# Optimization experiments

Measured on AMD Instinct MI355X. Metric: run time of the kernel, lower is better.

The kernel has to match this reference:

```python
import jax, jax.numpy as jnp
import numpy as np
from jax import lax

B, H, W, C = 64, 28, 28, 384
HEADS, WS, KD = 12, 7, 32        # head_dim = key_dim = 32, attn_ratio=1 -> d=32
DH = KD * HEADS                   # 384
NWIN = WS * WS                    # 49 tokens per window
MLP_H = 4 * C                     # 1536
L = H * W
EPS = 1e-5


def _layernorm(x, g, b):
    mu = jnp.mean(x, axis=-1, keepdims=True)
    var = jnp.var(x, axis=-1, keepdims=True)
    return (x - mu) * lax.rsqrt(var + EPS) * g + b


def setup_inputs() -> dict:
    key = jax.random.key(0)
    ks = jax.random.split(key, 16)
    w = lambda k, shape, s=0.02: (jax.random.normal(k, shape) * s).astype(jnp.float32)

    # relative-position bias index table, exactly as in Attention.__init__
    points = [(i, j) for i in range(WS) for j in range(WS)]
    offsets, idxs = {}, []
    for p1 in points:
        for p2 in points:
            off = (abs(p1[0] - p2[0]), abs(p1[1] - p2[1]))
            if off not in offsets:
                offsets[off] = len(offsets)
            idxs.append(offsets[off])
    bias_idxs = jnp.asarray(np.array(idxs, dtype=np.int32).reshape(NWIN, NWIN))

    return dict(
        x=jax.random.normal(ks[0], (B, L, C), dtype=jnp.float32),
        norm1_g=jnp.ones((C,), jnp.float32), norm1_b=jnp.zeros((C,), jnp.float32),
        qkv_w=w(ks[1], (DH + 2 * KD * HEADS, C)), qkv_b=jnp.zeros((DH + 2 * KD * HEADS,), jnp.float32),
        attn_bias=w(ks[2], (HEADS, len(offsets))),
        bias_idxs=bias_idxs,
        proj_w=w(ks[3], (C, DH)), proj_b=jnp.zeros((C,), jnp.float32),
        conv_w=w(ks[4], (C, 1, 3, 3)),  # depthwise, groups=C, no bias
        bn_g=jnp.ones((C,), jnp.float32), bn_b=jnp.zeros((C,), jnp.float32),
        bn_mean=jnp.zeros((C,), jnp.float32), bn_var=jnp.ones((C,), jnp.float32),
        norm2_g=jnp.ones((C,), jnp.float32), norm2_b=jnp.zeros((C,), jnp.float32),
        fc1_w=w(ks[5], (MLP_H, C)), fc1_b=jnp.zeros((MLP_H,), jnp.float32),
        fc2_w=w(ks[6], (C, MLP_H)), fc2_b=jnp.zeros((C,), jnp.float32),
    )


def reference(x, norm1_g, norm1_b, qkv_w, qkv_b, attn_bias, bias_idxs,
              proj_w, proj_b, conv_w, bn_g, bn_b, bn_mean, bn_var,
              norm2_g, norm2_b, fc1_w, fc1_b, fc2_w, fc2_b):
    scale = KD ** -0.5
    nH, nW = H // WS, W // WS
    res_x = x

    xw = x.reshape(B, nH, WS, nW, WS, C).transpose(0, 1, 3, 2, 4, 5)
    xw = xw.reshape(B * nH * nW, NWIN, C)  # [Bw, 49, C]

    # --- windowed attention with relative-position bias ---
    xn = _layernorm(xw, norm1_g, norm1_b)
    qkv = xn @ qkv_w.T + qkv_b                      # [Bw, 49, dh + 2*nh_kd]
    qkv = qkv.reshape(-1, NWIN, HEADS, 3 * KD).transpose(0, 2, 1, 3)
    q, k, v = qkv[..., :KD], qkv[..., KD:2 * KD], qkv[..., 2 * KD:]
    bias = attn_bias[:, bias_idxs]                  # [heads, 49, 49]
    attn = jnp.einsum('bhnd,bhmd->bhnm', q, k) * scale + bias
    attn = jax.nn.softmax(attn, axis=-1)
    out = jnp.einsum('bhnm,bhmd->bhnd', attn, v)    # [Bw, heads, 49, d]
    out = out.transpose(0, 2, 1, 3).reshape(-1, NWIN, DH)
    out = out @ proj_w.T + proj_b

    # --- window reverse ---
    out = out.reshape(B, nH, nW, WS, WS, C).transpose(0, 1, 3, 2, 4, 5)
    out = out.reshape(B, L, C)

    x = res_x + out

    # --- depthwise conv 3x3 + BN (eval stats) ---
    xc = x.transpose(0, 2, 1).reshape(B, C, H, W)
    y = lax.conv_general_dilated(xc, conv_w, (1, 1), 'SAME',
                                 dimension_numbers=('NCHW', 'OIHW', 'NCHW'),
                                 feature_group_count=C)
    y = (y - bn_mean[:, None, None]) * lax.rsqrt(bn_var[:, None, None] + EPS)
    y = y * bn_g[:, None, None] + bn_b[:, None, None]
    x = y.reshape(B, C, L).transpose(0, 2, 1)

    # --- MLP with pre-LN ---
    h = _layernorm(x, norm2_g, norm2_b)
    h = jax.nn.gelu(h @ fc1_w.T + fc1_b, approximate=False)
    h = h @ fc2_w.T + fc2_b
    return x + h
```

## Files before the change

### kernel.cpp

```cpp
#include <hip/hip_runtime.h>
#include <hip/hip_bf16.h>
#include <math.h>

#define CDIM 384
#define NW 49
#define NHEADS 12
#define HDIM 32
#define LROW 784
#define NROWS 50176
#define MLPH 1536
#define QKVD 1152
#define MHALF 25088

typedef __hip_bfloat16 bf16;
typedef __attribute__((ext_vector_type(8))) short bf16x8;
typedef __attribute__((ext_vector_type(4))) short short4v;
typedef __attribute__((ext_vector_type(4))) float f32x4;

__device__ __forceinline__ float b2f(bf16 v) { return __bfloat162float(v); }
__device__ __forceinline__ bf16 f2b(float v) { return __float2bfloat16(v); }
__device__ __forceinline__ unsigned short fbits(float v) {
  bf16 t = f2b(v);
  return *(unsigned short*)&t;
}

__global__ __launch_bounds__(256) void k_fill(float* out, int n, float val) {
  int i = blockIdx.x * 256 + threadIdx.x;
  if (i < n) out[i] = val;
}

__global__ __launch_bounds__(256) void k_f2b(const float* __restrict__ in,
                                             bf16* __restrict__ out, int n) {
  int i = blockIdx.x * 256 + threadIdx.x;
  if (i < n) out[i] = f2b(in[i]);
}

__global__ __launch_bounds__(256) void k_ln_win(const float* __restrict__ in,
                                                const float* __restrict__ g,
                                                const float* __restrict__ b,
                                                bf16* __restrict__ outp) {
  __shared__ float s1[256], s2[256];
  const int tid = threadIdx.x;
  const int rg = blockIdx.x;
  const float* row = in + (size_t)rg * CDIM;
  float a = row[tid];
  float c2 = (tid < CDIM - 256) ? row[tid + 256] : 0.f;
  s1[tid] = a + c2;
  s2[tid] = a * a + c2 * c2;
  __syncthreads();
  for (int s = 128; s > 0; s >>= 1) {
    if (tid < s) { s1[tid] += s1[tid + s]; s2[tid] += s2[tid + s]; }
    __syncthreads();
  }
  const float mean = s1[0] * (1.f / CDIM);
  const float var = s2[0] * (1.f / CDIM) - mean * mean;
  const float inv = rsqrtf(var + 1e-5f);
  int bb = rg / LROW, l = rg - bb * LROW;
  int hs = l / 28, ws = l - hs * 28;
  int wi = hs / 7, r7 = hs - wi * 7, wj = ws / 7, s7 = ws - wj * 7;
  int wrow = (bb * 16 + wi * 4 + wj) * NW + r7 * 7 + s7;
  bf16* orow = outp + (size_t)wrow * CDIM;
  orow[tid] = f2b((row[tid] - mean) * inv * g[tid] + b[tid]);
  if (tid < CDIM - 256)
    orow[tid + 256] = f2b((row[tid + 256] - mean) * inv * g[tid + 256] + b[tid + 256]);
}

template<int K>
__device__ __forceinline__ void gemm_tile(const bf16* __restrict__ A,
                                          const bf16* __restrict__ W,
                                          int arow0, int brow0, f32x4 acc[4][4]) {
  __shared__ __align__(16) unsigned short As[128][40];
  __shared__ __align__(16) unsigned short Bs[128][40];
  const int tid = threadIdx.x;
  const int lane = tid & 63;
  const int wid = tid >> 6;
  const int wr = wid >> 1, wc = wid & 1;
  const int fr = lane & 15, kg = lane >> 4;
  const int r0 = tid >> 2, kc0 = (tid & 3) * 8;
  const int r1 = r0 + 64;
  for (int kt = 0; kt < K; kt += 32) {
    bf16x8 a0 = *(const bf16x8*)(A + (size_t)(arow0 + r0) * K + kt + kc0);
    bf16x8 a1 = *(const bf16x8*)(A + (size_t)(arow0 + r1) * K + kt + kc0);
    bf16x8 b0 = *(const bf16x8*)(W + (size_t)(brow0 + r0) * K + kt + kc0);
    bf16x8 b1 = *(const bf16x8*)(W + (size_t)(brow0 + r1) * K + kt + kc0);
    if (kt) __syncthreads();
    *(bf16x8*)(&As[r0][kc0]) = a0;
    *(bf16x8*)(&As[r1][kc0]) = a1;
    *(bf16x8*)(&Bs[r0][kc0]) = b0;
    *(bf16x8*)(&Bs[r1][kc0]) = b1;
    __syncthreads();
    bf16x8 af[4], bv[4];
#pragma unroll
    for (int i = 0; i < 4; ++i) {
      af[i] = *(const bf16x8*)(&As[wr * 64 + i * 16 + fr][kg * 8]);
      bv[i] = *(const bf16x8*)(&Bs[wc * 64 + i * 16 + fr][kg * 8]);
    }
#pragma unroll
    for (int i = 0; i < 4; ++i)
#pragma unroll
      for (int j = 0; j < 4; ++j)
        acc[i][j] = __builtin_amdgcn_mfma_f32_16x16x32_bf16(af[i], bv[j], acc[i][j], 0, 0, 0);
  }
}

#define GEMM_PROLOGUE(KK)                                                   \
  f32x4 acc[4][4];                                                          \
  for (int i = 0; i < 4; ++i)                                               \
    for (int j = 0; j < 4; ++j) acc[i][j] = (f32x4){0.f, 0.f, 0.f, 0.f};    \
  const int arow0 = blockIdx.x * 128, bcol0 = blockIdx.y * 128;             \
  gemm_tile<KK>(A, W, arow0, bcol0, acc);                                   \
  const int tid = threadIdx.x, lane = tid & 63, wid = tid >> 6;             \
  const int wr = wid >> 1, wc = wid & 1, fr = lane & 15, rq = lane >> 4;

__global__ __launch_bounds__(256) void k_gqkv(const bf16* __restrict__ A,
                                              const bf16* __restrict__ W,
                                              const float* __restrict__ bias,
                                              bf16* __restrict__ out) {
  GEMM_PROLOGUE(CDIM)
#pragma unroll
  for (int i = 0; i < 4; ++i)
#pragma unroll
    for (int r = 0; r < 4; ++r) {
      int m = arow0 + wr * 64 + i * 16 + rq * 4 + r;
#pragma unroll
      for (int j = 0; j < 4; ++j) {
        int n = bcol0 + wc * 64 + j * 16 + fr;
        out[(size_t)m * QKVD + n] = f2b(acc[i][j][r] + bias[n]);
      }
    }
}

__global__ __launch_bounds__(256) void k_gproj(const bf16* __restrict__ A,
                                               const bf16* __restrict__ W,
                                               const float* __restrict__ bias,
                                               const float* __restrict__ xin,
                                               float* __restrict__ x1) {
  GEMM_PROLOGUE(CDIM)
#pragma unroll
  for (int i = 0; i < 4; ++i)
#pragma unroll
    for (int r = 0; r < 4; ++r) {
      int m = arow0 + wr * 64 + i * 16 + rq * 4 + r;
      int win = m / NW, nn = m - win * NW;
      int bb = win >> 4, wrem = win & 15, wi = wrem >> 2, wj = wrem & 3;
      int r7 = nn / 7, s7 = nn - r7 * 7;
      int l = (wi * 7 + r7) * 28 + wj * 7 + s7;
      size_t srow = (size_t)(bb * LROW + l) * CDIM;
#pragma unroll
      for (int j = 0; j < 4; ++j) {
        int n = bcol0 + wc * 64 + j * 16 + fr;
        x1[srow + n] = xin[srow + n] + acc[i][j][r] + bias[n];
      }
    }
}

__global__ __launch_bounds__(256) void k_gfc1(const bf16* __restrict__ A,
                                              const bf16* __restrict__ W,
                                              const float* __restrict__ bias,
                                              bf16* __restrict__ out) {
  GEMM_PROLOGUE(CDIM)
#pragma unroll
  for (int i = 0; i < 4; ++i)
#pragma unroll
    for (int r = 0; r < 4; ++r) {
      int m = arow0 + wr * 64 + i * 16 + rq * 4 + r;
#pragma unroll
      for (int j = 0; j < 4; ++j) {
        int n = bcol0 + wc * 64 + j * 16 + fr;
        float v = acc[i][j][r] + bias[n];
        out[(size_t)m * MLPH + n] = f2b(0.5f * v * (1.f + erff(v * 0.70710678118654752f)));
      }
    }
}

__global__ __launch_bounds__(256) void k_gfc2(const bf16* __restrict__ A,
                                              const bf16* __restrict__ W,
                                              const float* __restrict__ bias,
                                              float* __restrict__ xout) {
  GEMM_PROLOGUE(MLPH)
#pragma unroll
  for (int i = 0; i < 4; ++i)
#pragma unroll
    for (int r = 0; r < 4; ++r) {
      int m = arow0 + wr * 64 + i * 16 + rq * 4 + r;
#pragma unroll
      for (int j = 0; j < 4; ++j) {
        int n = bcol0 + wc * 64 + j * 16 + fr;
        size_t dst = (size_t)m * CDIM + n;
        xout[dst] = xout[dst] + acc[i][j][r] + bias[n];
      }
    }
}

__global__ __launch_bounds__(256) void k_attn2(const bf16* __restrict__ qkv,
                                               const float* __restrict__ attn_bias,
                                               const int* __restrict__ bias_idxs,
                                               int noff, bf16* __restrict__ outp) {
  __shared__ __align__(16) unsigned short Psh[4][64][72];
  const int tid = threadIdx.x;
  const int wid = tid >> 6, lane = tid & 63;
  const int fr = lane & 15, kg = lane >> 4;
  const int gid = blockIdx.x * 4 + wid;
  const int win = gid / NHEADS, h = gid - win * NHEADS;
  const bf16* base = qkv + (size_t)win * NW * QKVD + h * 96;

  const bf16x8 zero8 = {0, 0, 0, 0, 0, 0, 0, 0};
  bf16x8 qf[4], kf[4];
#pragma unroll
  for (int i = 0; i < 4; ++i) {
    int rr = i * 16 + fr;
    qf[i] = (rr < NW) ? *(const bf16x8*)(base + (size_t)rr * QKVD + kg * 8) : zero8;
    kf[i] = (rr < NW) ? *(const bf16x8*)(base + (size_t)rr * QKVD + 32 + kg * 8) : zero8;
  }
  f32x4 s[4][4];
#pragma unroll
  for (int i = 0; i < 4; ++i)
#pragma unroll
    for (int j = 0; j < 4; ++j)
      s[i][j] = (f32x4){0.f, 0.f, 0.f, 0.f};
#pragma unroll
  for (int i = 0; i < 4; ++i)
#pragma unroll
    for (int j = 0; j < 4; ++j)
      s[i][j] = __builtin_amdgcn_mfma_f32_16x16x32_bf16(qf[i], kf[j], s[i][j], 0, 0, 0);

  const float scale = 0.17677669529663687f;
  float rsum[4][4];
#pragma unroll
  for (int i = 0; i < 4; ++i)
#pragma unroll
    for (int r = 0; r < 4; ++r) {
      int n = i * 16 + kg * 4 + r;
      int nc = (n < NW) ? n : NW - 1;
      float mx = -1e30f;
#pragma unroll
      for (int j = 0; j < 4; ++j) {
        int mcol = j * 16 + fr;
        float v = (mcol < NW)
                      ? s[i][j][r] * scale + attn_bias[h * noff + bias_idxs[nc * NW + mcol]]
                      : -1e30f;
        s[i][j][r] = v;
        mx = fmaxf(mx, v);
      }
#pragma unroll
      for (int msk = 1; msk < 16; msk <<= 1) mx = fmaxf(mx, __shfl_xor(mx, msk));
      float sum = 0.f;
#pragma unroll
      for (int j = 0; j < 4; ++j) {
        float e = __expf(s[i][j][r] - mx);
        s[i][j][r] = e;
        sum += e;
      }
#pragma unroll
      for (int msk = 1; msk < 16; msk <<= 1) sum += __shfl_xor(sum, msk);
      rsum[i][r] = sum;
    }

#pragma unroll
  for (int i = 0; i < 4; ++i)
#pragma unroll
    for (int r = 0; r < 4; ++r) {
      int n = i * 16 + kg * 4 + r;
#pragma unroll
      for (int j = 0; j < 4; ++j) {
        Psh[wid][n][j * 16 + fr] = fbits(s[i][j][r]);
      }
    }
  __syncthreads();

  bf16x8 vf[2][2];
#pragma unroll
  for (int j = 0; j < 2; ++j)
#pragma unroll
    for (int kt = 0; kt < 2; ++kt)
#pragma unroll
      for (int e = 0; e < 8; ++e) {
        int m = kt * 32 + kg * 8 + e;
        bf16 val = (m < NW) ? base[(size_t)m * QKVD + 64 + j * 16 + fr] : f2b(0.f);
        vf[j][kt][e] = *(short*)&val;
      }

  f32x4 o[4][2];
#pragma unroll
  for (int i = 0; i < 4; ++i)
#pragma unroll
    for (int j = 0; j < 2; ++j) o[i][j] = (f32x4){0.f, 0.f, 0.f, 0.f};
#pragma unroll
  for (int kt = 0; kt < 2; ++kt) {
    bf16x8 pa[4];
#pragma unroll
    for (int i = 0; i < 4; ++i)
      pa[i] = *(const bf16x8*)(&Psh[wid][i * 16 + fr][kt * 32 + kg * 8]);
#pragma unroll
    for (int i = 0; i < 4; ++i)
#pragma unroll
      for (int j = 0; j < 2; ++j)
        o[i][j] = __builtin_amdgcn_mfma_f32_16x16x32_bf16(pa[i], vf[j][kt], o[i][j], 0, 0, 0);
  }

#pragma unroll
  for (int i = 0; i < 4; ++i)
#pragma unroll
    for (int r = 0; r < 4; ++r) {
      int n = i * 16 + kg * 4 + r;
      if (n < NW) {
        float inv = 1.f / rsum[i][r];
        bf16* orow = outp + ((size_t)win * NW + n) * CDIM + h * HDIM;
#pragma unroll
        for (int j = 0; j < 2; ++j) orow[j * 16 + fr] = f2b(o[i][j][r] * inv);
      }
    }
}

__global__ __launch_bounds__(384) void k_convln(const float* __restrict__ x1,
                                                const float* __restrict__ cw,
                                                const float* __restrict__ bng,
                                                const float* __restrict__ bnb,
                                                const float* __restrict__ bnm,
                                                const float* __restrict__ bnv,
                                                const float* __restrict__ lng,
                                                const float* __restrict__ lnb,
                                                float* __restrict__ x2,
                                                bf16* __restrict__ xn2) {
  __shared__ float wT[9][CDIM];
  __shared__ float ls1[4][96], ls2[4][96];
  const int tid = threadIdx.x;
#pragma unroll
  for (int i = 0; i < 9; ++i) {
    int fidx = i * 384 + tid;
    wT[fidx % 9][fidx / 9] = cw[fidx];
  }
  __syncthreads();
  const int ri = tid / 96, j = tid - ri * 96;
  const int rg = blockIdx.x * 4 + ri;
  const int b = rg / LROW, l = rg - b * LROW;
  const int h = l / 28, w = l - h * 28;
  const int c0 = j * 4;
  f32x4 acc = {0.f, 0.f, 0.f, 0.f};
#pragma unroll
  for (int dh = -1; dh <= 1; ++dh) {
    int hh = h + dh;
    if (hh < 0 || hh >= 28) continue;
#pragma unroll
    for (int dw = -1; dw <= 1; ++dw) {
      int ww = w + dw;
      if (ww < 0 || ww >= 28) continue;
      f32x4 xi = *(const f32x4*)(x1 + ((size_t)b * LROW + hh * 28 + ww) * CDIM + c0);
      const float* wt = &wT[(dh + 1) * 3 + (dw + 1)][c0];
      acc[0] += xi[0] * wt[0];
      acc[1] += xi[1] * wt[1];
      acc[2] += xi[2] * wt[2];
      acc[3] += xi[3] * wt[3];
    }
  }
  f32x4 m4 = *(const f32x4*)(bnm + c0), v4 = *(const f32x4*)(bnv + c0);
  f32x4 g4 = *(const f32x4*)(bng + c0), b4 = *(const f32x4*)(bnb + c0);
  f32x4 y;
#pragma unroll
  for (int e = 0; e < 4; ++e)
    y[e] = (acc[e] - m4[e]) * rsqrtf(v4[e] + 1e-5f) * g4[e] + b4[e];
  *(f32x4*)(x2 + (size_t)rg * CDIM + c0) = y;
  ls1[ri][j] = y[0] + y[1] + y[2] + y[3];
  ls2[ri][j] = y[0] * y[0] + y[1] * y[1] + y[2] * y[2] + y[3] * y[3];
  __syncthreads();
  if (j < 32) {
    ls1[ri][j] += ls1[ri][j + 32] + ls1[ri][j + 64];
    ls2[ri][j] += ls2[ri][j + 32] + ls2[ri][j + 64];
  }
  __syncthreads();
  for (int s = 16; s > 0; s >>= 1) {
    if (j < s) { ls1[ri][j] += ls1[ri][j + s]; ls2[ri][j] += ls2[ri][j + s]; }
    __syncthreads();
  }
  const float mean = ls1[ri][0] * (1.f / CDIM);
  const float var = ls2[ri][0] * (1.f / CDIM) - mean * mean;
  const float inv = rsqrtf(var + 1e-5f);
  f32x4 lg = *(const f32x4*)(lng + c0), lb = *(const f32x4*)(lnb + c0);
  short4v ov;
#pragma unroll
  for (int e = 0; e < 4; ++e)
    ov[e] = (short)fbits((y[e] - mean) * inv * lg[e] + lb[e]);
  *(short4v*)((unsigned short*)xn2 + (size_t)rg * CDIM + c0) = ov;
}

extern "C" void kernel_launch(void* const* d_in, const int* in_sizes, int n_in,
                              void* d_out, int out_size, void* d_ws, size_t ws_size,
                              hipStream_t stream) {
  float* out = (float*)d_out;
  static const int EXP[20] = {19267584, 384, 384, 442368, 1152, 588, 2401, 147456, 384, 3456,
                              384, 384, 384, 384, 384, 384, 589824, 1536, 589824, 384};
  const void* p[20];
  bool ok = (n_in == 20);
  int badslot = 30;
  if (ok) {
    bool used[20] = {false};
    for (int i = 0; i < 20 && ok; ++i) {
      int occ = 0;
      for (int j = 0; j < i; ++j) if (EXP[j] == EXP[i]) ++occ;
      int found = -1, seen = 0;
      for (int j = 0; j < 20; ++j) {
        if (in_sizes[j] == EXP[i]) {
          if (seen == occ) { found = j; break; }
          ++seen;
        }
      }
      if (found < 0 || used[found]) { ok = false; badslot = i; break; }
      used[found] = true;
      p[i] = d_in[found];
    }
  }
  const int NOUT = NROWS * CDIM;
  if (!ok) {
    k_fill<<<(NOUT + 255) / 256, 256, 0, stream>>>(out, NOUT, -(2.0f + 0.05f * badslot));
    return;
  }
  const size_t RB = (size_t)NROWS * CDIM;
  if (ws_size < RB * 8 + 1024) {
    k_fill<<<(NOUT + 255) / 256, 256, 0, stream>>>(out, NOUT, -5.0f);
    return;
  }
  char* base = (char*)d_ws;
  bf16* xn1 = (bf16*)base;
  bf16* qkvb = (bf16*)(base + RB * 2);
  bf16* attnb = (bf16*)base;
  float* x1 = (float*)(base + RB * 2);
  bf16* wfc1 = (bf16*)(base + RB * 6);
  bf16* wfc2 = (bf16*)(base + RB * 6 + 1179648);
  bf16* xn2 = (bf16*)base;
  bf16* hbuf = (bf16*)(base + RB * 2);
  bf16* wqkv = (bf16*)d_out;
  bf16* wproj = (bf16*)d_out + 442368;

  const float* xin = (const float*)p[0];
  const int noff = 49;

  k_f2b<<<(442368 + 255) / 256, 256, 0, stream>>>((const float*)p[3], wqkv, 442368);
  k_f2b<<<(147456 + 255) / 256, 256, 0, stream>>>((const float*)p[7], wproj, 147456);

  k_ln_win<<<NROWS, 256, 0, stream>>>(xin, (const float*)p[1], (const float*)p[2], xn1);
  {
    dim3 g(NROWS / 128, QKVD / 128);
    k_gqkv<<<g, 256, 0, stream>>>(xn1, wqkv, (const float*)p[4], qkvb);
  }
  k_attn2<<<(1024 * NHEADS) / 4, 256, 0, stream>>>(
      qkvb, (const float*)p[5], (const int*)p[6], noff, attnb);
  k_f2b<<<(589824 + 255) / 256, 256, 0, stream>>>((const float*)p[16], wfc1, 589824);
  k_f2b<<<(589824 + 255) / 256, 256, 0, stream>>>((const float*)p[18], wfc2, 589824);
  {
    dim3 g(NROWS / 128, CDIM / 128);
    k_gproj<<<g, 256, 0, stream>>>(attnb, wproj, (const float*)p[8], xin, x1);
  }
  k_convln<<<NROWS / 4, 384, 0, stream>>>(
      x1, (const float*)p[9], (const float*)p[10], (const float*)p[11],
      (const float*)p[12], (const float*)p[13], (const float*)p[14],
      (const float*)p[15], out, xn2);
  {
    dim3 g1(MHALF / 128, MLPH / 128), g2(MHALF / 128, CDIM / 128);
    k_gfc1<<<g1, 256, 0, stream>>>(xn2, wfc1, (const float*)p[17], hbuf);
    k_gfc2<<<g2, 256, 0, stream>>>(hbuf, wfc2, (const float*)p[19], out);
    k_gfc1<<<g1, 256, 0, stream>>>(xn2 + (size_t)MHALF * CDIM, wfc1, (const float*)p[17], hbuf);
    k_gfc2<<<g2, 256, 0, stream>>>(hbuf, wfc2, (const float*)p[19], out + (size_t)MHALF * CDIM);
  }
}
```

Measured before the change: 823.3 us.

## Load GEMM tiles directly to LDS with XOR swizzle and K-step 64

Replaces register-staged global-to-LDS copies in the shared GEMM tile with global_load_lds direct-to-LDS transfers. It doubles the K tile to 64 and uses an XOR-swizzled unpadded LDS layout to avoid bank conflicts on fragment reads. The goal is to cut VGPR pressure and instruction count in the load path and halve the number of barriers per K. The risk is that the swizzle has to match exactly between the writer lanes and the reader slots. There is also still no double buffering, so load latency stays exposed.

```diff
diff --git a/kernel.cpp b/kernel.cpp
--- a/kernel.cpp
+++ b/kernel.cpp
@@ -69,37 +69,42 @@
 __device__ __forceinline__ void gemm_tile(const bf16* __restrict__ A,
                                           const bf16* __restrict__ W,
                                           int arow0, int brow0, f32x4 acc[4][4]) {
-  __shared__ __align__(16) unsigned short As[128][40];
-  __shared__ __align__(16) unsigned short Bs[128][40];
+  __shared__ __align__(16) unsigned short As[128 * 64];
+  __shared__ __align__(16) unsigned short Bs[128 * 64];
   const int tid = threadIdx.x;
   const int lane = tid & 63;
   const int wid = tid >> 6;
   const int wr = wid >> 1, wc = wid & 1;
   const int fr = lane & 15, kg = lane >> 4;
-  const int r0 = tid >> 2, kc0 = (tid & 3) * 8;
-  const int r1 = r0 + 64;
-  for (int kt = 0; kt < K; kt += 32) {
-    bf16x8 a0 = *(const bf16x8*)(A + (size_t)(arow0 + r0) * K + kt + kc0);
-    bf16x8 a1 = *(const bf16x8*)(A + (size_t)(arow0 + r1) * K + kt + kc0);
-    bf16x8 b0 = *(const bf16x8*)(W + (size_t)(brow0 + r0) * K + kt + kc0);
-    bf16x8 b1 = *(const bf16x8*)(W + (size_t)(brow0 + r1) * K + kt + kc0);
+  const int srow = wid * 32 + (lane >> 3);
+  const int scol = (((lane & 7) ^ ((lane >> 3) & 7)) * 8);
+  for (int kt = 0; kt < K; kt += 64) {
     if (kt) __syncthreads();
-    *(bf16x8*)(&As[r0][kc0]) = a0;
-    *(bf16x8*)(&As[r1][kc0]) = a1;
-    *(bf16x8*)(&Bs[r0][kc0]) = b0;
-    *(bf16x8*)(&Bs[r1][kc0]) = b1;
+#pragma unroll
+    for (int i = 0; i < 4; ++i) {
+      __builtin_amdgcn_global_load_lds(
+          (const __attribute__((address_space(1))) void*)(A + (size_t)(arow0 + srow + i * 8) * K + kt + scol),
+          (__attribute__((address_space(3))) void*)(&As[(wid * 32 + i * 8) * 64]), 16, 0, 0);
+      __builtin_amdgcn_global_load_lds(
+          (const __attribute__((address_space(1))) void*)(W + (size_t)(brow0 + srow + i * 8) * K + kt + scol),
+          (__attribute__((address_space(3))) void*)(&Bs[(wid * 32 + i * 8) * 64]), 16, 0, 0);
+    }
     __syncthreads();
-    bf16x8 af[4], bv[4];
-#pragma unroll
-    for (int i = 0; i < 4; ++i) {
-      af[i] = *(const bf16x8*)(&As[wr * 64 + i * 16 + fr][kg * 8]);
-      bv[i] = *(const bf16x8*)(&Bs[wc * 64 + i * 16 + fr][kg * 8]);
-    }
-#pragma unroll
-    for (int i = 0; i < 4; ++i)
-#pragma unroll
-      for (int j = 0; j < 4; ++j)
-        acc[i][j] = __builtin_amdgcn_mfma_f32_16x16x32_bf16(af[i], bv[j], acc[i][j], 0, 0, 0);
+#pragma unroll
+    for (int kk = 0; kk < 2; ++kk) {
+      const int slot = ((kk * 4 + kg) ^ (fr & 7)) * 8;
+      bf16x8 af[4], bv[4];
+#pragma unroll
+      for (int i = 0; i < 4; ++i) {
+        af[i] = *(const bf16x8*)(&As[(wr * 64 + i * 16 + fr) * 64 + slot]);
+        bv[i] = *(const bf16x8*)(&Bs[(wc * 64 + i * 16 + fr) * 64 + slot]);
+      }
+#pragma unroll
+      for (int i = 0; i < 4; ++i)
+#pragma unroll
+        for (int j = 0; j < 4; ++j)
+          acc[i][j] = __builtin_amdgcn_mfma_f32_16x16x32_bf16(af[i], bv[j], acc[i][j], 0, 0, 0);
+    }
   }
 }
 
```

Result: faster. 747.0 us (-9.3%).
